# Kernel tuning notes

Measured on AMD Instinct MI355X. Metric: run time of the kernel, lower is better.

## Reference

```python
import jax, jax.numpy as jnp
import numpy as np

N = 512          # num_satellites
STATE_DIM = 6    # pos(3) + vel(3)
OBJ_DIM = 58
F = STATE_DIM + OBJ_DIM          # node feature dim = 64
HID = (128, 64, 32)
EDGE_IN = 2 * F + 1              # sender + receiver + distance
NODE_IN = F + HID[-1]            # node feats + aggregated messages


def _linear_init(key, d_in, d_out):
    kw, _ = jax.random.split(key)
    w = jax.random.normal(kw, (d_in, d_out), jnp.float32) / np.sqrt(d_in).astype(np.float32)
    b = jnp.zeros((d_out,), jnp.float32)
    return w, b


def setup_inputs() -> dict:
    key = jax.random.key(0)
    ks = jax.random.split(key, 12)
    ew0, eb0 = _linear_init(ks[0], EDGE_IN, HID[0])
    ew1, eb1 = _linear_init(ks[1], HID[0], HID[1])
    ew2, eb2 = _linear_init(ks[2], HID[1], HID[2])
    nw0, nb0 = _linear_init(ks[3], NODE_IN, HID[0])
    nw1, nb1 = _linear_init(ks[4], HID[0], HID[1])
    nw2, nb2 = _linear_init(ks[5], HID[1], HID[2])
    nwo, nbo = _linear_init(ks[6], HID[2], F)   # residual projection back to F
    rw, rb = _linear_init(ks[7], F, 3)          # control readout
    states = jax.random.normal(ks[8], (N, STATE_DIM), jnp.float32)
    objectives = jax.random.normal(ks[9], (OBJ_DIM,), jnp.float32)
    return dict(states=states, objectives=objectives,
                ew0=ew0, eb0=eb0, ew1=ew1, eb1=eb1, ew2=ew2, eb2=eb2,
                nw0=nw0, nb0=nb0, nw1=nw1, nb1=nb1, nw2=nw2, nb2=nb2,
                nwo=nwo, nbo=nbo, rw=rw, rb=rb,
                num_message_passing=3)


def _edge_index(n):
    ii, jj = np.meshgrid(np.arange(n), np.arange(n), indexing='ij')
    m = ii != jj
    return jnp.asarray(ii[m]), jnp.asarray(jj[m])  # sender i, receiver j; E = n*(n-1)


def reference(states, objectives, ew0, eb0, ew1, eb1, ew2, eb2,
              nw0, nb0, nw1, nb1, nw2, nb2, nwo, nbo, rw, rb,
              num_message_passing):
    n = states.shape[0]
    snd, rcv = _edge_index(n)
    # node features: state concat broadcast objectives -> [N, F]
    nf = jnp.concatenate(
        [states, jnp.broadcast_to(objectives, (n, objectives.shape[0]))], axis=-1)
    # distances from raw states (constant across iterations): [E, 1]
    rel = states[rcv, :3] - states[snd, :3]
    dist = jnp.linalg.norm(rel, axis=-1, keepdims=True)
    relu = jax.nn.relu
    for _ in range(num_message_passing):
        # edge MLP over all E edges: [E, 2F+1] -> [E, 32]
        x = jnp.concatenate([nf[snd], nf[rcv], dist], axis=-1)
        h = relu(x @ ew0 + eb0)
        h = relu(h @ ew1 + eb1)
        msg = relu(h @ ew2 + eb2)
        # sum-aggregate incoming messages at receiver j: [N, 32]
        agg = jax.ops.segment_sum(msg, rcv, num_segments=n)
        # node MLP + residual: [N, F+32] -> [N, F]
        y = jnp.concatenate([nf, agg], axis=-1)
        h = relu(y @ nw0 + nb0)
        h = relu(h @ nw1 + nb1)
        h = relu(h @ nw2 + nb2)
        nf = nf + h @ nwo + nbo
    # control readout: [N, 3]
    return nf @ rw + rb
```

## Files before the change

kernel.cpp:

```cpp
#include <hip/hip_runtime.h>
#include <math.h>

#define NSAT 512
#define FDIM 64
#define H0D  128
#define H1D  64
#define H2D  32
#define KP1  68
#define ROWS 256

#define WS_NF    0
#define WS_PSA   (WS_NF  + NSAT * FDIM)
#define WS_PRA   (WS_PSA + NSAT * H0D)
#define WS_PSB   (WS_PRA + NSAT * H0D)
#define WS_PRB   (WS_PSB + NSAT * H0D)
#define WS_WT    (WS_PRB + NSAT * H0D)

using short8_t = __attribute__((ext_vector_type(8))) short;
using short4_t = __attribute__((ext_vector_type(4))) short;
using int4_t   = __attribute__((ext_vector_type(4))) int;
using int2_t   = __attribute__((ext_vector_type(2))) int;
using floatx4  = __attribute__((ext_vector_type(4))) float;
using floatx16 = __attribute__((ext_vector_type(16))) float;

__device__ __forceinline__ void split_ru(float x, short& hi, short& lo) {
    unsigned u = __builtin_bit_cast(unsigned, x);
    unsigned hb = (u + 0x8000u) >> 16;
    hi = (short)hb;
    float r = x - __builtin_bit_cast(float, hb << 16);
    lo = (short)((__builtin_bit_cast(unsigned, r) + 0x8000u) >> 16);
}

__device__ __forceinline__ void split8_pk(const float* __restrict__ v,
                                          short8_t& bh, short8_t& bl) {
    unsigned t[8]; unsigned ru[8];
    #pragma unroll
    for (int e = 0; e < 8; ++e) {
        unsigned u = __builtin_bit_cast(unsigned, v[e]);
        t[e] = u + 0x8000u;
        float r = v[e] - __builtin_bit_cast(float, t[e] & 0xffff0000u);
        ru[e] = __builtin_bit_cast(unsigned, r);
    }
    int4_t hv, lv;
    #pragma unroll
    for (int p = 0; p < 4; ++p) {
        hv[p] = (int)__builtin_amdgcn_perm(t[2*p+1],  t[2*p],  0x07060302u);
        lv[p] = (int)__builtin_amdgcn_perm(ru[2*p+1], ru[2*p], 0x07060302u);
    }
    bh = __builtin_bit_cast(short8_t, hv);
    bl = __builtin_bit_cast(short8_t, lv);
}

__device__ __forceinline__ void split4_pk(const float* __restrict__ v,
                                          short4_t& h, short4_t& l) {
    unsigned t[4]; unsigned ru[4];
    #pragma unroll
    for (int e = 0; e < 4; ++e) {
        unsigned u = __builtin_bit_cast(unsigned, v[e]);
        t[e] = u + 0x8000u;
        float r = v[e] - __builtin_bit_cast(float, t[e] & 0xffff0000u);
        ru[e] = __builtin_bit_cast(unsigned, r);
    }
    int2_t hv, lv;
    #pragma unroll
    for (int p = 0; p < 2; ++p) {
        hv[p] = (int)__builtin_amdgcn_perm(t[2*p+1],  t[2*p],  0x07060302u);
        lv[p] = (int)__builtin_amdgcn_perm(ru[2*p+1], ru[2*p], 0x07060302u);
    }
    h = __builtin_bit_cast(short4_t, hv);
    l = __builtin_bit_cast(short4_t, lv);
}

__device__ __forceinline__ void compute_pre(const float* __restrict__ nfl,
                                            const float* __restrict__ ew0,
                                            const float* __restrict__ eb0,
                                            int i, int t,
                                            float* __restrict__ preSA,
                                            float* __restrict__ preR) {
    if (t < H0D) {
        int k = t;
        float s0 = 0.f, s1 = 0.f, s2 = 0.f, s3 = 0.f;
        #pragma unroll
        for (int f = 0; f < FDIM; f += 4) {
            s0 = fmaf(nfl[f + 0], ew0[(f + 0) * H0D + k], s0);
            s1 = fmaf(nfl[f + 1], ew0[(f + 1) * H0D + k], s1);
            s2 = fmaf(nfl[f + 2], ew0[(f + 2) * H0D + k], s2);
            s3 = fmaf(nfl[f + 3], ew0[(f + 3) * H0D + k], s3);
        }
        int kk = (k >> 3) & 7, lhi = k >> 6, jj = k & 7;
        preSA[((i >> 5) * 8 + kk) * 512 + (lhi * 32 + (i & 31)) * 8 + jj] =
            (s0 + s1) + (s2 + s3);
    } else if (t < 2 * H0D) {
        int k = t - H0D;
        float s0 = eb0[k], s1 = 0.f, s2 = 0.f, s3 = 0.f;
        #pragma unroll
        for (int f = 0; f < FDIM; f += 4) {
            s0 = fmaf(nfl[f + 0], ew0[(FDIM + f + 0) * H0D + k], s0);
            s1 = fmaf(nfl[f + 1], ew0[(FDIM + f + 1) * H0D + k], s1);
            s2 = fmaf(nfl[f + 2], ew0[(FDIM + f + 2) * H0D + k], s2);
            s3 = fmaf(nfl[f + 3], ew0[(FDIM + f + 3) * H0D + k], s3);
        }
        preR[i * H0D + k] = (s0 + s1) + (s2 + s3);
    }
}

__global__ void setup_kernel(const float* __restrict__ states,
                             const float* __restrict__ objectives,
                             const float* __restrict__ ew0,
                             const float* __restrict__ eb0,
                             const float* __restrict__ ew1,
                             const float* __restrict__ ew2,
                             float* __restrict__ nf,
                             float* __restrict__ preSA,
                             float* __restrict__ preR,
                             short* __restrict__ w1A_hi,
                             short* __restrict__ w1A_lo,
                             short* __restrict__ w2t_hi,
                             short* __restrict__ w2t_lo) {
    __shared__ float nfl[FDIM];
    int b = blockIdx.x, t = threadIdx.x;
    if (b < NSAT) {
        if (t < FDIM) {
            float v = (t < 6) ? states[b * 6 + t] : objectives[t - 6];
            nfl[t] = v;
            nf[b * FDIM + t] = v;
        }
        __syncthreads();
        compute_pre(nfl, ew0, eb0, b, t, preSA, preR);
    } else {
        int e = (b - NSAT) * 256 + t;
        if (e < H1D * H0D) {
            int jj = e & 7;
            int l  = (e >> 3) & 63;
            int kk = (e >> 9) & 7;
            int mh = e >> 12;
            int m = mh * 32 + (l & 31);
            int k = (l >> 5) * 64 + kk * 8 + jj;
            short hi, lo; split_ru(ew1[k * H1D + m], hi, lo);
            w1A_hi[e] = hi; w1A_lo[e] = lo;
        } else if (e < H1D * H0D + H2D * H1D) {
            int e2 = e - H1D * H0D;
            int c = e2 >> 6, k = e2 & 63;
            short hi, lo; split_ru(ew2[k * H2D + c], hi, lo);
            w2t_hi[e2] = hi; w2t_lo[e2] = lo;
        }
    }
}

__global__ __launch_bounds__(512, 2)
void edge_node_kernel(const float* __restrict__ states,
                      const float* __restrict__ preSA,
                      const float* __restrict__ preR,
                      const float* __restrict__ ew0,
                      const float* __restrict__ eb0,
                      const float* __restrict__ eb1,
                      const float* __restrict__ eb2,
                      const short* __restrict__ w1A_hi,
                      const short* __restrict__ w1A_lo,
                      const short* __restrict__ w2t_hi,
                      const short* __restrict__ w2t_lo,
                      const float* __restrict__ nw0, const float* __restrict__ nb0,
                      const float* __restrict__ nw1, const float* __restrict__ nb1,
                      const float* __restrict__ nw2, const float* __restrict__ nb2,
                      const float* __restrict__ nwo, const float* __restrict__ nbo,
                      const float* __restrict__ rw,  const float* __restrict__ rb,
                      float* __restrict__ nf,
                      float* __restrict__ preSA_w,
                      float* __restrict__ preR_w,
                      float* __restrict__ out,
                      int final_iter) {
    extern __shared__ __align__(16) short h1_dyn[];
    short* h1_hi = h1_dyn;
    short* h1_lo = h1_dyn + ROWS * KP1;

    __shared__ __align__(16) float preR_l[H0D];
    __shared__ __align__(16) float wd_l[H0D];
    __shared__ __align__(16) float eb1_l[H1D];
    __shared__ float eb2_l[H2D];
    __shared__ __align__(16) float red_l[8 * H2D];
    __shared__ float y_l[96];
    __shared__ float hA_l[H0D];
    __shared__ float hB_l[H1D];
    __shared__ float hC_l[H2D];
    __shared__ float nfl2[FDIM];

    int t = threadIdx.x, j = blockIdx.x;
    int w = t >> 6, lane = t & 63;
    int lhi = lane >> 5, llo = lane & 31;

    if (t < H0D)                          preR_l[t] = preR[j * H0D + t];
    else if (t < 2 * H0D)                 wd_l[t - H0D] = ew0[H0D * H0D + (t - H0D)];
    else if (t < 2 * H0D + H1D)           eb1_l[t - 2 * H0D] = eb1[t - 2 * H0D];
    else if (t < 2 * H0D + H1D + H2D)     eb2_l[t - 2 * H0D - H1D] = eb2[t - 2 * H0D - H1D];
    __syncthreads();

    float rjx = states[j * 6 + 0];
    float rjy = states[j * 6 + 1];
    float rjz = states[j * 6 + 2];

    int s_loc = w * 32 + llo;
    const short* pAh0 = w1A_hi + lane * 8;
    const short* pAl0 = w1A_lo + lane * 8;

    int lq = lane >> 4, l15 = lane & 15;
    const short* pA2h0 = w2t_hi + l15 * H1D + lq * 8;
    const short* pA2l0 = w2t_lo + l15 * H1D + lq * 8;
    const short* pA2h1 = w2t_hi + (16 + l15) * H1D + lq * 8;
    const short* pA2l1 = w2t_lo + (16 + l15) * H1D + lq * 8;
    int boA = (w * 32 + l15) * KP1 + lq * 8;
    int boB = boA + 16 * KP1;

    float racc[8];
    #pragma unroll
    for (int r = 0; r < 8; ++r) racc[r] = 0.f;

    #pragma unroll 1
    for (int P = 0; P < 2; ++P) {
        int s_glb = P * ROWS + s_loc;
        float dx = states[s_glb * 6 + 0] - rjx;
        float dy = states[s_glb * 6 + 1] - rjy;
        float dz = states[s_glb * 6 + 2] - rjz;
        float d = sqrtf(dx * dx + dy * dy + dz * dz);

        const float* pS = preSA + (size_t)((P * 8 + w) * 8) * 512 + lane * 8;

        floatx16 accA, accB;
        #pragma unroll
        for (int r = 0; r < 16; ++r) { accA[r] = 0.f; accB[r] = 0.f; }

        #pragma unroll
        for (int kk = 0; kk < 8; ++kk) {
            float4 a0 = *(const float4*)(pS + kk * 512);
            float4 a1 = *(const float4*)(pS + kk * 512 + 4);
            int kb = lhi * 64 + kk * 8;
            float4 r0 = *(const float4*)&preR_l[kb];
            float4 r1 = *(const float4*)&preR_l[kb + 4];
            float4 q0 = *(const float4*)&wd_l[kb];
            float4 q1 = *(const float4*)&wd_l[kb + 4];
            float v[8];
            v[0] = fmaxf(a0.x + fmaf(d, q0.x, r0.x), 0.f);
            v[1] = fmaxf(a0.y + fmaf(d, q0.y, r0.y), 0.f);
            v[2] = fmaxf(a0.z + fmaf(d, q0.z, r0.z), 0.f);
            v[3] = fmaxf(a0.w + fmaf(d, q0.w, r0.w), 0.f);
            v[4] = fmaxf(a1.x + fmaf(d, q1.x, r1.x), 0.f);
            v[5] = fmaxf(a1.y + fmaf(d, q1.y, r1.y), 0.f);
            v[6] = fmaxf(a1.z + fmaf(d, q1.z, r1.z), 0.f);
            v[7] = fmaxf(a1.w + fmaf(d, q1.w, r1.w), 0.f);
            short8_t bh, bl;
            split8_pk(v, bh, bl);
            short8_t ah0 = *(const short8_t*)(pAh0 + kk * 512);
            short8_t al0 = *(const short8_t*)(pAl0 + kk * 512);
            short8_t ah1 = *(const short8_t*)(pAh0 + 4096 + kk * 512);
            short8_t al1 = *(const short8_t*)(pAl0 + 4096 + kk * 512);
            accA = __builtin_amdgcn_mfma_f32_32x32x16_bf16(ah0, bh, accA, 0, 0, 0);
            accA = __builtin_amdgcn_mfma_f32_32x32x16_bf16(ah0, bl, accA, 0, 0, 0);
            accA = __builtin_amdgcn_mfma_f32_32x32x16_bf16(al0, bh, accA, 0, 0, 0);
            accB = __builtin_amdgcn_mfma_f32_32x32x16_bf16(ah1, bh, accB, 0, 0, 0);
            accB = __builtin_amdgcn_mfma_f32_32x32x16_bf16(ah1, bl, accB, 0, 0, 0);
            accB = __builtin_amdgcn_mfma_f32_32x32x16_bf16(al1, bh, accB, 0, 0, 0);
        }

        asm volatile("s_waitcnt lgkmcnt(0)" ::: "memory");

        {
            #pragma unroll
            for (int mh = 0; mh < 2; ++mh) {
                #pragma unroll
                for (int q = 0; q < 4; ++q) {
                    int m0 = mh * 32 + q * 8 + lhi * 4;
                    float vv[4];
                    #pragma unroll
                    for (int r = 0; r < 4; ++r) {
                        float c = mh ? accB[q * 4 + r] : accA[q * 4 + r];
                        vv[r] = fmaxf(c + eb1_l[m0 + r], 0.f);
                    }
                    short4_t ph, pl;
                    split4_pk(vv, ph, pl);
                    *(short4_t*)&h1_hi[s_loc * KP1 + m0] = ph;
                    *(short4_t*)&h1_lo[s_loc * KP1 + m0] = pl;
                }
            }
        }

        floatx4 aA0, aA1, aB0, aB1;
        #pragma unroll
        for (int r = 0; r < 4; ++r) { aA0[r]=0.f; aA1[r]=0.f; aB0[r]=0.f; aB1[r]=0.f; }
        #pragma unroll
        for (int kk = 0; kk < 2; ++kk) {
            short4_t b0, b1, c0, c1;
            b0 = *(const short4_t*)&h1_hi[boA + kk * 32];
            b1 = *(const short4_t*)&h1_hi[boA + kk * 32 + 4];
            c0 = *(const short4_t*)&h1_lo[boA + kk * 32];
            c1 = *(const short4_t*)&h1_lo[boA + kk * 32 + 4];
            short8_t bhA = __builtin_shufflevector(b0, b1, 0,1,2,3,4,5,6,7);
            short8_t blA = __builtin_shufflevector(c0, c1, 0,1,2,3,4,5,6,7);
            b0 = *(const short4_t*)&h1_hi[boB + kk * 32];
            b1 = *(const short4_t*)&h1_hi[boB + kk * 32 + 4];
            c0 = *(const short4_t*)&h1_lo[boB + kk * 32];
            c1 = *(const short4_t*)&h1_lo[boB + kk * 32 + 4];
            short8_t bhB = __builtin_shufflevector(b0, b1, 0,1,2,3,4,5,6,7);
            short8_t blB = __builtin_shufflevector(c0, c1, 0,1,2,3,4,5,6,7);
            short8_t a0h = *(const short8_t*)(pA2h0 + kk * 32);
            short8_t a0l = *(const short8_t*)(pA2l0 + kk * 32);
            short8_t a1h = *(const short8_t*)(pA2h1 + kk * 32);
            short8_t a1l = *(const short8_t*)(pA2l1 + kk * 32);
            aA0 = __builtin_amdgcn_mfma_f32_16x16x32_bf16(a0h, bhA, aA0, 0, 0, 0);
            aA0 = __builtin_amdgcn_mfma_f32_16x16x32_bf16(a0h, blA, aA0, 0, 0, 0);
            aA0 = __builtin_amdgcn_mfma_f32_16x16x32_bf16(a0l, bhA, aA0, 0, 0, 0);
            aA1 = __builtin_amdgcn_mfma_f32_16x16x32_bf16(a1h, bhA, aA1, 0, 0, 0);
            aA1 = __builtin_amdgcn_mfma_f32_16x16x32_bf16(a1h, blA, aA1, 0, 0, 0);
            aA1 = __builtin_amdgcn_mfma_f32_16x16x32_bf16(a1l, bhA, aA1, 0, 0, 0);
            aB0 = __builtin_amdgcn_mfma_f32_16x16x32_bf16(a0h, bhB, aB0, 0, 0, 0);
            aB0 = __builtin_amdgcn_mfma_f32_16x16x32_bf16(a0h, blB, aB0, 0, 0, 0);
            aB0 = __builtin_amdgcn_mfma_f32_16x16x32_bf16(a0l, bhB, aB0, 0, 0, 0);
            aB1 = __builtin_amdgcn_mfma_f32_16x16x32_bf16(a1h, bhB, aB1, 0, 0, 0);
            aB1 = __builtin_amdgcn_mfma_f32_16x16x32_bf16(a1h, blB, aB1, 0, 0, 0);
            aB1 = __builtin_amdgcn_mfma_f32_16x16x32_bf16(a1l, bhB, aB1, 0, 0, 0);
        }

        {
            bool selfA = (P * ROWS + w * 32 + l15 == j);
            bool selfB = (P * ROWS + w * 32 + 16 + l15 == j);
            #pragma unroll
            for (int r = 0; r < 4; ++r) {
                float vA = fmaxf(aA0[r] + eb2_l[lq * 4 + r], 0.f);
                float vB = fmaxf(aB0[r] + eb2_l[lq * 4 + r], 0.f);
                if (selfA) vA = 0.f;
                if (selfB) vB = 0.f;
                racc[r] += vA + vB;
                float wA = fmaxf(aA1[r] + eb2_l[16 + lq * 4 + r], 0.f);
                float wB = fmaxf(aB1[r] + eb2_l[16 + lq * 4 + r], 0.f);
                if (selfA) wA = 0.f;
                if (selfB) wB = 0.f;
                racc[4 + r] += wA + wB;
            }
        }
    }

    {
        #pragma unroll
        for (int r = 0; r < 8; ++r) {
            float v = racc[r];
            v += __shfl_xor(v, 1, 64); v += __shfl_xor(v, 2, 64);
            v += __shfl_xor(v, 4, 64); v += __shfl_xor(v, 8, 64);
            racc[r] = v;
        }
        if (l15 == 0) {
            *(float4*)&red_l[w * H2D + lq * 4] =
                make_float4(racc[0], racc[1], racc[2], racc[3]);
            *(float4*)&red_l[w * H2D + 16 + lq * 4] =
                make_float4(racc[4], racc[5], racc[6], racc[7]);
        }
    }
    __syncthreads();

    if (t < FDIM) y_l[t] = nf[j * FDIM + t];
    else if (t < 96) {
        int c = t - FDIM;
        float s = 0.f;
        #pragma unroll
        for (int gg = 0; gg < 8; ++gg) s += red_l[gg * H2D + c];
        y_l[t] = s;
    }
    __syncthreads();
    if (t < H0D) {
        float s0 = nb0[t], s1 = 0.f, s2 = 0.f, s3 = 0.f;
        #pragma unroll
        for (int f = 0; f < 96; f += 4) {
            s0 = fmaf(y_l[f + 0], nw0[(f + 0) * H0D + t], s0);
            s1 = fmaf(y_l[f + 1], nw0[(f + 1) * H0D + t], s1);
            s2 = fmaf(y_l[f + 2], nw0[(f + 2) * H0D + t], s2);
            s3 = fmaf(y_l[f + 3], nw0[(f + 3) * H0D + t], s3);
        }
        hA_l[t] = fmaxf((s0 + s1) + (s2 + s3), 0.f);
    }
    __syncthreads();
    if (t < H1D) {
        float s0 = nb1[t], s1 = 0.f, s2 = 0.f, s3 = 0.f;
        #pragma unroll
        for (int k = 0; k < H0D; k += 4) {
            s0 = fmaf(hA_l[k + 0], nw1[(k + 0) * H1D + t], s0);
            s1 = fmaf(hA_l[k + 1], nw1[(k + 1) * H1D + t], s1);
            s2 = fmaf(hA_l[k + 2], nw1[(k + 2) * H1D + t], s2);
            s3 = fmaf(hA_l[k + 3], nw1[(k + 3) * H1D + t], s3);
        }
        hB_l[t] = fmaxf((s0 + s1) + (s2 + s3), 0.f);
    }
    __syncthreads();
    if (t < H2D) {
        float s0 = nb2[t], s1 = 0.f, s2 = 0.f, s3 = 0.f;
        #pragma unroll
        for (int m = 0; m < H1D; m += 4) {
            s0 = fmaf(hB_l[m + 0], nw2[(m + 0) * H2D + t], s0);
            s1 = fmaf(hB_l[m + 1], nw2[(m + 1) * H2D + t], s1);
            s2 = fmaf(hB_l[m + 2], nw2[(m + 2) * H2D + t], s2);
            s3 = fmaf(hB_l[m + 3], nw2[(m + 3) * H2D + t], s3);
        }
        hC_l[t] = fmaxf((s0 + s1) + (s2 + s3), 0.f);
    }
    __syncthreads();
    if (t < FDIM) {
        float s = nbo[t];
        #pragma unroll
        for (int c = 0; c < H2D; ++c) s = fmaf(hC_l[c], nwo[c * FDIM + t], s);
        float v = y_l[t] + s;
        nfl2[t] = v;
        if (!final_iter) nf[j * FDIM + t] = v;
    }
    __syncthreads();
    if (final_iter) {
        if (t < 3) {
            float s0 = rb[t], s1 = 0.f, s2 = 0.f, s3 = 0.f;
            #pragma unroll
            for (int f = 0; f < FDIM; f += 4) {
                s0 = fmaf(nfl2[f + 0], rw[(f + 0) * 3 + t], s0);
                s1 = fmaf(nfl2[f + 1], rw[(f + 1) * 3 + t], s1);
                s2 = fmaf(nfl2[f + 2], rw[(f + 2) * 3 + t], s2);
                s3 = fmaf(nfl2[f + 3], rw[(f + 3) * 3 + t], s3);
            }
            out[j * 3 + t] = (s0 + s1) + (s2 + s3);
        }
    } else {
        compute_pre(nfl2, ew0, eb0, j, t, preSA_w, preR_w);
    }
}

extern "C" void kernel_launch(void* const* d_in, const int* in_sizes, int n_in,
                              void* d_out, int out_size, void* d_ws, size_t ws_size,
                              hipStream_t stream) {
    const float* states     = (const float*)d_in[0];
    const float* objectives = (const float*)d_in[1];
    const float* ew0 = (const float*)d_in[2];
    const float* eb0 = (const float*)d_in[3];
    const float* ew1 = (const float*)d_in[4];
    const float* eb1 = (const float*)d_in[5];
    const float* ew2 = (const float*)d_in[6];
    const float* eb2 = (const float*)d_in[7];
    const float* nw0 = (const float*)d_in[8];
    const float* nb0 = (const float*)d_in[9];
    const float* nw1 = (const float*)d_in[10];
    const float* nb1 = (const float*)d_in[11];
    const float* nw2 = (const float*)d_in[12];
    const float* nb2 = (const float*)d_in[13];
    const float* nwo = (const float*)d_in[14];
    const float* nbo = (const float*)d_in[15];
    const float* rw  = (const float*)d_in[16];
    const float* rb  = (const float*)d_in[17];
    float* out = (float*)d_out;
    float* ws  = (float*)d_ws;

    float* nf      = ws + WS_NF;
    float* preSA_a = ws + WS_PSA;
    float* preR_a  = ws + WS_PRA;
    float* preSA_b = ws + WS_PSB;
    float* preR_b  = ws + WS_PRB;
    short* w1A_hi = (short*)(ws + WS_WT);
    short* w1A_lo = w1A_hi + H1D * H0D;
    short* w2t_hi = w1A_lo + H1D * H0D;
    short* w2t_lo = w2t_hi + H2D * H1D;

    const int dyn_lds = 2 * ROWS * KP1 * (int)sizeof(short);
    static bool attr_set = false;
    if (!attr_set) {
        hipFuncSetAttribute((const void*)edge_node_kernel,
                            hipFuncAttributeMaxDynamicSharedMemorySize, dyn_lds);
        attr_set = true;
    }

    setup_kernel<<<NSAT + 40, 256, 0, stream>>>(states, objectives, ew0, eb0,
                                                ew1, ew2, nf, preSA_a, preR_a,
                                                w1A_hi, w1A_lo, w2t_hi, w2t_lo);
    for (int it = 0; it < 3; ++it) {
        const float* pS_r = (it & 1) ? preSA_b : preSA_a;
        const float* pR_r = (it & 1) ? preR_b  : preR_a;
        float* pS_w = (it & 1) ? preSA_a : preSA_b;
        float* pR_w = (it & 1) ? preR_a  : preR_b;
        edge_node_kernel<<<NSAT, 512, dyn_lds, stream>>>(
            states, pS_r, pR_r, ew0, eb0, eb1, eb2,
            w1A_hi, w1A_lo, w2t_hi, w2t_lo,
            nw0, nb0, nw1, nb1, nw2, nb2, nwo, nbo, rw, rb,
            nf, pS_w, pR_w, out, (it == 2) ? 1 : 0);
    }
}
```

Before: 198.1 us.

## Process 64 senders per wave in one pass to reuse weight fragments

Drops the two-pass loop over sender halves. Each wave now handles 64 sender rows at once, with doubled MFMA accumulators for both edge-MLP layers, so every weight fragment loaded is reused across two sender tiles and independent MFMAs are interleaved. The shared h1 buffer doubles to cover all 512 rows and launch bounds drop to one block per CU. That raises register and LDS pressure and cuts residency, which may serialize the 512-block grid across CUs.

```diff
diff --git a/kernel.cpp b/kernel.cpp
--- a/kernel.cpp
+++ b/kernel.cpp
@@ -7,7 +7,7 @@
 #define H1D  64
 #define H2D  32
 #define KP1  68
-#define ROWS 256
+#define ROWS 512
 
 #define WS_NF    0
 #define WS_PSA   (WS_NF  + NSAT * FDIM)
@@ -147,7 +147,7 @@
     }
 }
 
-__global__ __launch_bounds__(512, 2)
+__global__ __launch_bounds__(512, 1)
 void edge_node_kernel(const float* __restrict__ states,
                       const float* __restrict__ preSA,
                       const float* __restrict__ preR,
@@ -198,142 +198,205 @@
     float rjy = states[j * 6 + 1];
     float rjz = states[j * 6 + 2];
 
-    int s_loc = w * 32 + llo;
+    int s0r = w * 64 + llo;
+    int s1r = s0r + 32;
+    float dx0 = states[s0r * 6 + 0] - rjx;
+    float dy0 = states[s0r * 6 + 1] - rjy;
+    float dz0 = states[s0r * 6 + 2] - rjz;
+    float d0 = sqrtf(dx0 * dx0 + dy0 * dy0 + dz0 * dz0);
+    float dx1 = states[s1r * 6 + 0] - rjx;
+    float dy1 = states[s1r * 6 + 1] - rjy;
+    float dz1 = states[s1r * 6 + 2] - rjz;
+    float d1 = sqrtf(dx1 * dx1 + dy1 * dy1 + dz1 * dz1);
+
     const short* pAh0 = w1A_hi + lane * 8;
     const short* pAl0 = w1A_lo + lane * 8;
+    const float* pS0 = preSA + (size_t)((2 * w + 0) * 8) * 512 + lane * 8;
+    const float* pS1 = preSA + (size_t)((2 * w + 1) * 8) * 512 + lane * 8;
+
+    floatx16 accA0, accB0, accA1, accB1;
+    #pragma unroll
+    for (int r = 0; r < 16; ++r) {
+        accA0[r] = 0.f; accB0[r] = 0.f; accA1[r] = 0.f; accB1[r] = 0.f;
+    }
+
+    #pragma unroll
+    for (int kk = 0; kk < 8; ++kk) {
+        int kb = lhi * 64 + kk * 8;
+        float4 r0 = *(const float4*)&preR_l[kb];
+        float4 r1 = *(const float4*)&preR_l[kb + 4];
+        float4 q0 = *(const float4*)&wd_l[kb];
+        float4 q1 = *(const float4*)&wd_l[kb + 4];
+        float4 a0 = *(const float4*)(pS0 + kk * 512);
+        float4 a1 = *(const float4*)(pS0 + kk * 512 + 4);
+        float v0[8];
+        v0[0] = fmaxf(a0.x + fmaf(d0, q0.x, r0.x), 0.f);
+        v0[1] = fmaxf(a0.y + fmaf(d0, q0.y, r0.y), 0.f);
+        v0[2] = fmaxf(a0.z + fmaf(d0, q0.z, r0.z), 0.f);
+        v0[3] = fmaxf(a0.w + fmaf(d0, q0.w, r0.w), 0.f);
+        v0[4] = fmaxf(a1.x + fmaf(d0, q1.x, r1.x), 0.f);
+        v0[5] = fmaxf(a1.y + fmaf(d0, q1.y, r1.y), 0.f);
+        v0[6] = fmaxf(a1.z + fmaf(d0, q1.z, r1.z), 0.f);
+        v0[7] = fmaxf(a1.w + fmaf(d0, q1.w, r1.w), 0.f);
+        short8_t bh0, bl0;
+        split8_pk(v0, bh0, bl0);
+        float4 b0 = *(const float4*)(pS1 + kk * 512);
+        float4 b1 = *(const float4*)(pS1 + kk * 512 + 4);
+        float v1[8];
+        v1[0] = fmaxf(b0.x + fmaf(d1, q0.x, r0.x), 0.f);
+        v1[1] = fmaxf(b0.y + fmaf(d1, q0.y, r0.y), 0.f);
+        v1[2] = fmaxf(b0.z + fmaf(d1, q0.z, r0.z), 0.f);
+        v1[3] = fmaxf(b0.w + fmaf(d1, q0.w, r0.w), 0.f);
+        v1[4] = fmaxf(b1.x + fmaf(d1, q1.x, r1.x), 0.f);
+        v1[5] = fmaxf(b1.y + fmaf(d1, q1.y, r1.y), 0.f);
+        v1[6] = fmaxf(b1.z + fmaf(d1, q1.z, r1.z), 0.f);
+        v1[7] = fmaxf(b1.w + fmaf(d1, q1.w, r1.w), 0.f);
+        short8_t bh1, bl1;
+        split8_pk(v1, bh1, bl1);
+        short8_t ah0 = *(const short8_t*)(pAh0 + kk * 512);
+        short8_t al0 = *(const short8_t*)(pAl0 + kk * 512);
+        short8_t ah1 = *(const short8_t*)(pAh0 + 4096 + kk * 512);
+        short8_t al1 = *(const short8_t*)(pAl0 + 4096 + kk * 512);
+        accA0 = __builtin_amdgcn_mfma_f32_32x32x16_bf16(ah0, bh0, accA0, 0, 0, 0);
+        accA1 = __builtin_amdgcn_mfma_f32_32x32x16_bf16(ah0, bh1, accA1, 0, 0, 0);
+        accB0 = __builtin_amdgcn_mfma_f32_32x32x16_bf16(ah1, bh0, accB0, 0, 0, 0);
+        accB1 = __builtin_amdgcn_mfma_f32_32x32x16_bf16(ah1, bh1, accB1, 0, 0, 0);
+        accA0 = __builtin_amdgcn_mfma_f32_32x32x16_bf16(ah0, bl0, accA0, 0, 0, 0);
+        accA1 = __builtin_amdgcn_mfma_f32_32x32x16_bf16(ah0, bl1, accA1, 0, 0, 0);
+        accB0 = __builtin_amdgcn_mfma_f32_32x32x16_bf16(ah1, bl0, accB0, 0, 0, 0);
+        accB1 = __builtin_amdgcn_mfma_f32_32x32x16_bf16(ah1, bl1, accB1, 0, 0, 0);
+        accA0 = __builtin_amdgcn_mfma_f32_32x32x16_bf16(al0, bh0, accA0, 0, 0, 0);
+        accA1 = __builtin_amdgcn_mfma_f32_32x32x16_bf16(al0, bh1, accA1, 0, 0, 0);
+        accB0 = __builtin_amdgcn_mfma_f32_32x32x16_bf16(al1, bh0, accB0, 0, 0, 0);
+        accB1 = __builtin_amdgcn_mfma_f32_32x32x16_bf16(al1, bh1, accB1, 0, 0, 0);
+    }
+
+    #pragma unroll
+    for (int T = 0; T < 2; ++T) {
+        int srow = T ? s1r : s0r;
+        #pragma unroll
+        for (int mh = 0; mh < 2; ++mh) {
+            #pragma unroll
+            for (int q = 0; q < 4; ++q) {
+                int m0 = mh * 32 + q * 8 + lhi * 4;
+                float vv[4];
+                #pragma unroll
+                for (int r = 0; r < 4; ++r) {
+                    float c;
+                    if (T == 0) c = mh ? accB0[q * 4 + r] : accA0[q * 4 + r];
+                    else        c = mh ? accB1[q * 4 + r] : accA1[q * 4 + r];
+                    vv[r] = fmaxf(c + eb1_l[m0 + r], 0.f);
+                }
+                short4_t ph, pl;
+                split4_pk(vv, ph, pl);
+                *(short4_t*)&h1_hi[srow * KP1 + m0] = ph;
+                *(short4_t*)&h1_lo[srow * KP1 + m0] = pl;
+            }
+        }
+    }
 
     int lq = lane >> 4, l15 = lane & 15;
     const short* pA2h0 = w2t_hi + l15 * H1D + lq * 8;
     const short* pA2l0 = w2t_lo + l15 * H1D + lq * 8;
     const short* pA2h1 = w2t_hi + (16 + l15) * H1D + lq * 8;
     const short* pA2l1 = w2t_lo + (16 + l15) * H1D + lq * 8;
-    int boA = (w * 32 + l15) * KP1 + lq * 8;
-    int boB = boA + 16 * KP1;
+    int bo0 = (w * 64 + l15) * KP1 + lq * 8;
+    int bo1 = bo0 + 16 * KP1;
+    int bo2 = bo0 + 32 * KP1;
+    int bo3 = bo0 + 48 * KP1;
+
+    floatx4 aA0, aA1, aB0, aB1, aC0, aC1, aD0, aD1;
+    #pragma unroll
+    for (int r = 0; r < 4; ++r) {
+        aA0[r]=0.f; aA1[r]=0.f; aB0[r]=0.f; aB1[r]=0.f;
+        aC0[r]=0.f; aC1[r]=0.f; aD0[r]=0.f; aD1[r]=0.f;
+    }
+    #pragma unroll
+    for (int kk = 0; kk < 2; ++kk) {
+        short8_t a0h = *(const short8_t*)(pA2h0 + kk * 32);
+        short8_t a0l = *(const short8_t*)(pA2l0 + kk * 32);
+        short8_t a1h = *(const short8_t*)(pA2h1 + kk * 32);
+        short8_t a1l = *(const short8_t*)(pA2l1 + kk * 32);
+        short4_t u0, u1, c0, c1;
+        u0 = *(const short4_t*)&h1_hi[bo0 + kk * 32];
+        u1 = *(const short4_t*)&h1_hi[bo0 + kk * 32 + 4];
+        c0 = *(const short4_t*)&h1_lo[bo0 + kk * 32];
+        c1 = *(const short4_t*)&h1_lo[bo0 + kk * 32 + 4];
+        short8_t bhA = __builtin_shufflevector(u0, u1, 0,1,2,3,4,5,6,7);
+        short8_t blA = __builtin_shufflevector(c0, c1, 0,1,2,3,4,5,6,7);
+        u0 = *(const short4_t*)&h1_hi[bo1 + kk * 32];
+        u1 = *(const short4_t*)&h1_hi[bo1 + kk * 32 + 4];
+        c0 = *(const short4_t*)&h1_lo[bo1 + kk * 32];
+        c1 = *(const short4_t*)&h1_lo[bo1 + kk * 32 + 4];
+        short8_t bhB = __builtin_shufflevector(u0, u1, 0,1,2,3,4,5,6,7);
+        short8_t blB = __builtin_shufflevector(c0, c1, 0,1,2,3,4,5,6,7);
+        u0 = *(const short4_t*)&h1_hi[bo2 + kk * 32];
+        u1 = *(const short4_t*)&h1_hi[bo2 + kk * 32 + 4];
+        c0 = *(const short4_t*)&h1_lo[bo2 + kk * 32];
+        c1 = *(const short4_t*)&h1_lo[bo2 + kk * 32 + 4];
+        short8_t bhC = __builtin_shufflevector(u0, u1, 0,1,2,3,4,5,6,7);
+        short8_t blC = __builtin_shufflevector(c0, c1, 0,1,2,3,4,5,6,7);
+        u0 = *(const short4_t*)&h1_hi[bo3 + kk * 32];
+        u1 = *(const short4_t*)&h1_hi[bo3 + kk * 32 + 4];
+        c0 = *(const short4_t*)&h1_lo[bo3 + kk * 32];
+        c1 = *(const short4_t*)&h1_lo[bo3 + kk * 32 + 4];
+        short8_t bhD = __builtin_shufflevector(u0, u1, 0,1,2,3,4,5,6,7);
+        short8_t blD = __builtin_shufflevector(c0, c1, 0,1,2,3,4,5,6,7);
+
+        aA0 = __builtin_amdgcn_mfma_f32_16x16x32_bf16(a0h, bhA, aA0, 0, 0, 0);
+        aB0 = __builtin_amdgcn_mfma_f32_16x16x32_bf16(a0h, bhB, aB0, 0, 0, 0);
+        aC0 = __builtin_amdgcn_mfma_f32_16x16x32_bf16(a0h, bhC, aC0, 0, 0, 0);
+        aD0 = __builtin_amdgcn_mfma_f32_16x16x32_bf16(a0h, bhD, aD0, 0, 0, 0);
+        aA1 = __builtin_amdgcn_mfma_f32_16x16x32_bf16(a1h, bhA, aA1, 0, 0, 0);
+        aB1 = __builtin_amdgcn_mfma_f32_16x16x32_bf16(a1h, bhB, aB1, 0, 0, 0);
+        aC1 = __builtin_amdgcn_mfma_f32_16x16x32_bf16(a1h, bhC, aC1, 0, 0, 0);
+        aD1 = __builtin_amdgcn_mfma_f32_16x16x32_bf16(a1h, bhD, aD1, 0, 0, 0);
+        aA0 = __builtin_amdgcn_mfma_f32_16x16x32_bf16(a0h, blA, aA0, 0, 0, 0);
+        aB0 = __builtin_amdgcn_mfma_f32_16x16x32_bf16(a0h, blB, aB0, 0, 0, 0);
+        aC0 = __builtin_amdgcn_mfma_f32_16x16x32_bf16(a0h, blC, aC0, 0, 0, 0);
+        aD0 = __builtin_amdgcn_mfma_f32_16x16x32_bf16(a0h, blD, aD0, 0, 0, 0);
+        aA1 = __builtin_amdgcn_mfma_f32_16x16x32_bf16(a1h, blA, aA1, 0, 0, 0);
+        aB1 = __builtin_amdgcn_mfma_f32_16x16x32_bf16(a1h, blB, aB1, 0, 0, 0);
+        aC1 = __builtin_amdgcn_mfma_f32_16x16x32_bf16(a1h, blC, aC1, 0, 0, 0);
+        aD1 = __builtin_amdgcn_mfma_f32_16x16x32_bf16(a1h, blD, aD1, 0, 0, 0);
+        aA0 = __builtin_amdgcn_mfma_f32_16x16x32_bf16(a0l, bhA, aA0, 0, 0, 0);
+        aB0 = __builtin_amdgcn_mfma_f32_16x16x32_bf16(a0l, bhB, aB0, 0, 0, 0);
+        aC0 = __builtin_amdgcn_mfma_f32_16x16x32_bf16(a0l, bhC, aC0, 0, 0, 0);
+        aD0 = __builtin_amdgcn_mfma_f32_16x16x32_bf16(a0l, bhD, aD0, 0, 0, 0);
+        aA1 = __builtin_amdgcn_mfma_f32_16x16x32_bf16(a1l, bhA, aA1, 0, 0, 0);
+        aB1 = __builtin_amdgcn_mfma_f32_16x16x32_bf16(a1l, bhB, aB1, 0, 0, 0);
+        aC1 = __builtin_amdgcn_mfma_f32_16x16x32_bf16(a1l, bhC, aC1, 0, 0, 0);
+        aD1 = __builtin_amdgcn_mfma_f32_16x16x32_bf16(a1l, bhD, aD1, 0, 0, 0);
+    }
 
     float racc[8];
-    #pragma unroll
-    for (int r = 0; r < 8; ++r) racc[r] = 0.f;
-
-    #pragma unroll 1
-    for (int P = 0; P < 2; ++P) {
-        int s_glb = P * ROWS + s_loc;
-        float dx = states[s_glb * 6 + 0] - rjx;
-        float dy = states[s_glb * 6 + 1] - rjy;
-        float dz = states[s_glb * 6 + 2] - rjz;
-        float d = sqrtf(dx * dx + dy * dy + dz * dz);
-
-        const float* pS = preSA + (size_t)((P * 8 + w) * 8) * 512 + lane * 8;
-
-        floatx16 accA, accB;
-        #pragma unroll
-        for (int r = 0; r < 16; ++r) { accA[r] = 0.f; accB[r] = 0.f; }
-
-        #pragma unroll
-        for (int kk = 0; kk < 8; ++kk) {
-            float4 a0 = *(const float4*)(pS + kk * 512);
-            float4 a1 = *(const float4*)(pS + kk * 512 + 4);
-            int kb = lhi * 64 + kk * 8;
-            float4 r0 = *(const float4*)&preR_l[kb];
-            float4 r1 = *(const float4*)&preR_l[kb + 4];
-            float4 q0 = *(const float4*)&wd_l[kb];
-            float4 q1 = *(const float4*)&wd_l[kb + 4];
-            float v[8];
-            v[0] = fmaxf(a0.x + fmaf(d, q0.x, r0.x), 0.f);
-            v[1] = fmaxf(a0.y + fmaf(d, q0.y, r0.y), 0.f);
-            v[2] = fmaxf(a0.z + fmaf(d, q0.z, r0.z), 0.f);
-            v[3] = fmaxf(a0.w + fmaf(d, q0.w, r0.w), 0.f);
-            v[4] = fmaxf(a1.x + fmaf(d, q1.x, r1.x), 0.f);
-            v[5] = fmaxf(a1.y + fmaf(d, q1.y, r1.y), 0.f);
-            v[6] = fmaxf(a1.z + fmaf(d, q1.z, r1.z), 0.f);
-            v[7] = fmaxf(a1.w + fmaf(d, q1.w, r1.w), 0.f);
-            short8_t bh, bl;
-            split8_pk(v, bh, bl);
-            short8_t ah0 = *(const short8_t*)(pAh0 + kk * 512);
-            short8_t al0 = *(const short8_t*)(pAl0 + kk * 512);
-            short8_t ah1 = *(const short8_t*)(pAh0 + 4096 + kk * 512);
-            short8_t al1 = *(const short8_t*)(pAl0 + 4096 + kk * 512);
-            accA = __builtin_amdgcn_mfma_f32_32x32x16_bf16(ah0, bh, accA, 0, 0, 0);
-            accA = __builtin_amdgcn_mfma_f32_32x32x16_bf16(ah0, bl, accA, 0, 0, 0);
-            accA = __builtin_amdgcn_mfma_f32_32x32x16_bf16(al0, bh, accA, 0, 0, 0);
-            accB = __builtin_amdgcn_mfma_f32_32x32x16_bf16(ah1, bh, accB, 0, 0, 0);
-            accB = __builtin_amdgcn_mfma_f32_32x32x16_bf16(ah1, bl, accB, 0, 0, 0);
-            accB = __builtin_amdgcn_mfma_f32_32x32x16_bf16(al1, bh, accB, 0, 0, 0);
-        }
-
-        asm volatile("s_waitcnt lgkmcnt(0)" ::: "memory");
-
-        {
-            #pragma unroll
-            for (int mh = 0; mh < 2; ++mh) {
-                #pragma unroll
-                for (int q = 0; q < 4; ++q) {
-                    int m0 = mh * 32 + q * 8 + lhi * 4;
-                    float vv[4];
-                    #pragma unroll
-                    for (int r = 0; r < 4; ++r) {
-                        float c = mh ? accB[q * 4 + r] : accA[q * 4 + r];
-                        vv[r] = fmaxf(c + eb1_l[m0 + r], 0.f);
-                    }
-                    short4_t ph, pl;
-                    split4_pk(vv, ph, pl);
-                    *(short4_t*)&h1_hi[s_loc * KP1 + m0] = ph;
-                    *(short4_t*)&h1_lo[s_loc * KP1 + m0] = pl;
-                }
-            }
-        }
-
-        floatx4 aA0, aA1, aB0, aB1;
-        #pragma unroll
-        for (int r = 0; r < 4; ++r) { aA0[r]=0.f; aA1[r]=0.f; aB0[r]=0.f; aB1[r]=0.f; }
-        #pragma unroll
-        for (int kk = 0; kk < 2; ++kk) {
-            short4_t b0, b1, c0, c1;
-            b0 = *(const short4_t*)&h1_hi[boA + kk * 32];
-            b1 = *(const short4_t*)&h1_hi[boA + kk * 32 + 4];
-            c0 = *(const short4_t*)&h1_lo[boA + kk * 32];
-            c1 = *(const short4_t*)&h1_lo[boA + kk * 32 + 4];
-            short8_t bhA = __builtin_shufflevector(b0, b1, 0,1,2,3,4,5,6,7);
-            short8_t blA = __builtin_shufflevector(c0, c1, 0,1,2,3,4,5,6,7);
-            b0 = *(const short4_t*)&h1_hi[boB + kk * 32];
-            b1 = *(const short4_t*)&h1_hi[boB + kk * 32 + 4];
-            c0 = *(const short4_t*)&h1_lo[boB + kk * 32];
-            c1 = *(const short4_t*)&h1_lo[boB + kk * 32 + 4];
-            short8_t bhB = __builtin_shufflevector(b0, b1, 0,1,2,3,4,5,6,7);
-            short8_t blB = __builtin_shufflevector(c0, c1, 0,1,2,3,4,5,6,7);
-            short8_t a0h = *(const short8_t*)(pA2h0 + kk * 32);
-            short8_t a0l = *(const short8_t*)(pA2l0 + kk * 32);
-            short8_t a1h = *(const short8_t*)(pA2h1 + kk * 32);
-            short8_t a1l = *(const short8_t*)(pA2l1 + kk * 32);
-            aA0 = __builtin_amdgcn_mfma_f32_16x16x32_bf16(a0h, bhA, aA0, 0, 0, 0);
-            aA0 = __builtin_amdgcn_mfma_f32_16x16x32_bf16(a0h, blA, aA0, 0, 0, 0);
-            aA0 = __builtin_amdgcn_mfma_f32_16x16x32_bf16(a0l, bhA, aA0, 0, 0, 0);
-            aA1 = __builtin_amdgcn_mfma_f32_16x16x32_bf16(a1h, bhA, aA1, 0, 0, 0);
-            aA1 = __builtin_amdgcn_mfma_f32_16x16x32_bf16(a1h, blA, aA1, 0, 0, 0);
-            aA1 = __builtin_amdgcn_mfma_f32_16x16x32_bf16(a1l, bhA, aA1, 0, 0, 0);
-            aB0 = __builtin_amdgcn_mfma_f32_16x16x32_bf16(a0h, bhB, aB0, 0, 0, 0);
-            aB0 = __builtin_amdgcn_mfma_f32_16x16x32_bf16(a0h, blB, aB0, 0, 0, 0);
-            aB0 = __builtin_amdgcn_mfma_f32_16x16x32_bf16(a0l, bhB, aB0, 0, 0, 0);
-            aB1 = __builtin_amdgcn_mfma_f32_16x16x32_bf16(a1h, bhB, aB1, 0, 0, 0);
-            aB1 = __builtin_amdgcn_mfma_f32_16x16x32_bf16(a1h, blB, aB1, 0, 0, 0);
-            aB1 = __builtin_amdgcn_mfma_f32_16x16x32_bf16(a1l, bhB, aB1, 0, 0, 0);
-        }
-
-        {
-            bool selfA = (P * ROWS + w * 32 + l15 == j);
-            bool selfB = (P * ROWS + w * 32 + 16 + l15 == j);
-            #pragma unroll
-            for (int r = 0; r < 4; ++r) {
-                float vA = fmaxf(aA0[r] + eb2_l[lq * 4 + r], 0.f);
-                float vB = fmaxf(aB0[r] + eb2_l[lq * 4 + r], 0.f);
-                if (selfA) vA = 0.f;
-                if (selfB) vB = 0.f;
-                racc[r] += vA + vB;
-                float wA = fmaxf(aA1[r] + eb2_l[16 + lq * 4 + r], 0.f);
-                float wB = fmaxf(aB1[r] + eb2_l[16 + lq * 4 + r], 0.f);
-                if (selfA) wA = 0.f;
-                if (selfB) wB = 0.f;
-                racc[4 + r] += wA + wB;
-            }
+    {
+        bool selfA = (w * 64 +  0 + l15 == j);
+        bool selfB = (w * 64 + 16 + l15 == j);
+        bool selfC = (w * 64 + 32 + l15 == j);
+        bool selfD = (w * 64 + 48 + l15 == j);
+        #pragma unroll
+        for (int r = 0; r < 4; ++r) {
+            float e0 = eb2_l[lq * 4 + r];
+            float vA = fmaxf(aA0[r] + e0, 0.f);
+            float vB = fmaxf(aB0[r] + e0, 0.f);
+            float vC = fmaxf(aC0[r] + e0, 0.f);
+            float vD = fmaxf(aD0[r] + e0, 0.f);
+            if (selfA) vA = 0.f;
+            if (selfB) vB = 0.f;
+            if (selfC) vC = 0.f;
+            if (selfD) vD = 0.f;
+            racc[r] = (vA + vB) + (vC + vD);
+            float e1 = eb2_l[16 + lq * 4 + r];
+            float uA = fmaxf(aA1[r] + e1, 0.f);
+            float uB = fmaxf(aB1[r] + e1, 0.f);
+            float uC = fmaxf(aC1[r] + e1, 0.f);
+            float uD = fmaxf(aD1[r] + e1, 0.f);
+            if (selfA) uA = 0.f;
+            if (selfB) uB = 0.f;
+            if (selfC) uC = 0.f;
+            if (selfD) uD = 0.f;
+            racc[4 + r] = (uA + uB) + (uC + uD);
         }
     }
 
```

Result: faster. 191.2 us (-3.5%).
